# Kernel optimization log

Hardware: AMD Instinct MI355X
Metric: run time of the kernel (lower is better)

The kernel has to match this reference:

```python
import jax, jax.numpy as jnp
import numpy as np

N = 50000      # nodes
E = 400000     # edges
IN_DIM = 128
HID = 64
HEADS1 = 4
OUT_DIM = 64
NEG_SLOPE = 0.2


def _gat_layer(x, W, attn_l, attn_r, bias, src, dst, heads, out_feats):
    # x: [N, F_in]; W: [F_in, heads*out]; attn_l/attn_r: [heads, out]; bias: [heads*out]
    n = x.shape[0]
    feat = (x @ W).reshape(n, heads, out_feats)              # [N, H, D]
    el = jnp.sum(feat * attn_l, axis=-1)                     # [N, H]
    er = jnp.sum(feat * attn_r, axis=-1)                     # [N, H]
    e = jax.nn.leaky_relu(el[src] + er[dst], NEG_SLOPE)      # [E, H]
    # segment softmax over incoming edges per destination node
    emax = jax.ops.segment_max(e, dst, num_segments=n)       # [N, H]
    ex = jnp.exp(e - emax[dst])                              # [E, H]
    denom = jax.ops.segment_sum(ex, dst, num_segments=n)     # [N, H]
    alpha = ex / denom[dst]                                  # [E, H]
    msg = alpha[:, :, None] * feat[src]                      # [E, H, D]
    rst = jax.ops.segment_sum(msg, dst, num_segments=n)      # [N, H, D]
    return rst + bias.reshape(1, heads, out_feats)


def setup_inputs() -> dict:
    key = jax.random.key(0)
    ks = jax.random.split(key, 12)
    features = jax.random.normal(ks[0], (N, IN_DIM), dtype=jnp.float32)
    src = jax.random.randint(ks[1], (E,), 0, N, dtype=jnp.int32)
    dst = jax.random.randint(ks[2], (E,), 0, N, dtype=jnp.int32)
    s1 = 1.0 / np.sqrt(IN_DIM)
    s2 = 1.0 / np.sqrt(HEADS1 * HID)
    W1 = jax.random.normal(ks[3], (IN_DIM, HEADS1 * HID), dtype=jnp.float32) * s1
    attn_l1 = jax.random.normal(ks[4], (HEADS1, HID), dtype=jnp.float32) * 0.1
    attn_r1 = jax.random.normal(ks[5], (HEADS1, HID), dtype=jnp.float32) * 0.1
    b1 = jnp.zeros((HEADS1 * HID,), dtype=jnp.float32)
    W2 = jax.random.normal(ks[6], (HEADS1 * HID, OUT_DIM), dtype=jnp.float32) * s2
    attn_l2 = jax.random.normal(ks[7], (1, OUT_DIM), dtype=jnp.float32) * 0.1
    attn_r2 = jax.random.normal(ks[8], (1, OUT_DIM), dtype=jnp.float32) * 0.1
    b2 = jnp.zeros((OUT_DIM,), dtype=jnp.float32)
    return {"features": features, "src": src, "dst": dst,
            "W1": W1, "attn_l1": attn_l1, "attn_r1": attn_r1, "b1": b1,
            "W2": W2, "attn_l2": attn_l2, "attn_r2": attn_r2, "b2": b2}


def reference(features, src, dst, W1, attn_l1, attn_r1, b1, W2, attn_l2, attn_r2, b2):
    h = _gat_layer(features, W1, attn_l1, attn_r1, b1, src, dst, HEADS1, HID)  # [N, 4, 64]
    h = h.reshape(h.shape[0], -1)                                             # flatten heads
    h = _gat_layer(h, W2, attn_l2, attn_r2, b2, src, dst, 1, OUT_DIM)         # [N, 1, 64]
    return h
```

## Files before the change

### kernel.cpp

```cpp
#include <hip/hip_runtime.h>
#include <hip/hip_bf16.h>

#define N_NODES 50000
#define N_EDGES 400000
#define IN_DIM 128
#define HID 64
#define HEADS 4
#define L1_OUT (HEADS * HID)
#define OUT_DIM 64
#define NEG_SLOPE 0.2f
#define SCAN_B 256
#define HIST_B 1563

typedef short bf16x8 __attribute__((ext_vector_type(8)));
typedef float f32x4 __attribute__((ext_vector_type(4)));

__device__ __forceinline__ float leaky(float x) { return x > 0.f ? x : NEG_SLOPE * x; }

__device__ __forceinline__ unsigned short bfh(float x) {
    unsigned u = __float_as_uint(x);
    return (unsigned short)((u + 0x7fffu + ((u >> 16) & 1u)) >> 16);
}
__device__ __forceinline__ float fb(unsigned short h) {
    return __uint_as_float(((unsigned)h) << 16);
}

__device__ __forceinline__ int swzA(int u) {
    return u ^ (((u >> 6) & 7) ^ (((u >> 4) & 3) << 1));
}

__global__ void hist_wprep_kernel(const int* __restrict__ dst, int* __restrict__ cnt,
                                  const float* __restrict__ W1, const float* __restrict__ W2,
                                  unsigned short* __restrict__ W1fh, unsigned short* __restrict__ W1fl,
                                  unsigned short* __restrict__ W2fh, unsigned short* __restrict__ W2fl) {
    int bid = blockIdx.x;
    if (bid < HIST_B) {
        int e = bid * 256 + threadIdx.x;
        if (e < N_EDGES) atomicAdd(&cnt[dst[e]], 1);
        return;
    }
    int s = (bid - HIST_B) * 256 + threadIdx.x;
    if (s < 4096) {
        int lane = s & 63, ks = (s >> 6) & 3, ntile = s >> 8;
        int n = ntile * 16 + (lane & 15);
        int kb = ks * 32 + (lane >> 4) * 8;
#pragma unroll
        for (int j = 0; j < 8; ++j) {
            float w = W1[(kb + j) * L1_OUT + n];
            unsigned short h = bfh(w);
            W1fh[s * 8 + j] = h;
            W1fl[s * 8 + j] = bfh(w - fb(h));
        }
    } else if (s < 6144) {
        int s2 = s - 4096;
        int lane = s2 & 63, ks = (s2 >> 6) & 7, ntile = s2 >> 9;
        int n = ntile * 16 + (lane & 15);
        int kb = ks * 32 + (lane >> 4) * 8;
#pragma unroll
        for (int j = 0; j < 8; ++j) {
            float w = W2[(kb + j) * OUT_DIM + n];
            unsigned short h = bfh(w);
            W2fh[s2 * 8 + j] = h;
            W2fl[s2 * 8 + j] = bfh(w - fb(h));
        }
    }
}

__global__ void scanA_kernel(const int* __restrict__ cnt, int* __restrict__ texcl,
                             int* __restrict__ bsum) {
    __shared__ int sh[SCAN_B];
    int tid = threadIdx.x;
    int i = blockIdx.x * SCAN_B + tid;
    int v = (i < N_NODES) ? cnt[i] : 0;
    sh[tid] = v;
    __syncthreads();
    for (int off = 1; off < SCAN_B; off <<= 1) {
        int t = (tid >= off) ? sh[tid - off] : 0;
        __syncthreads();
        sh[tid] += t;
        __syncthreads();
    }
    if (i < N_NODES) texcl[i] = sh[tid] - v;
    if (tid == SCAN_B - 1) bsum[blockIdx.x] = sh[tid];
}

__global__ void scanB_kernel(const int* __restrict__ bsum, int* __restrict__ bexcl, int nb) {
    __shared__ int sh[SCAN_B];
    int tid = threadIdx.x;
    int v = (tid < nb) ? bsum[tid] : 0;
    sh[tid] = v;
    __syncthreads();
    for (int off = 1; off < SCAN_B; off <<= 1) {
        int t = (tid >= off) ? sh[tid - off] : 0;
        __syncthreads();
        sh[tid] += t;
        __syncthreads();
    }
    if (tid < nb) bexcl[tid] = sh[tid] - v;
}

__global__ void scanC_kernel(const int* __restrict__ texcl, const int* __restrict__ bexcl,
                             int* __restrict__ row) {
    int i = blockIdx.x * blockDim.x + threadIdx.x;
    if (i < N_NODES) row[i] = texcl[i] + bexcl[i >> 8];
    if (blockIdx.x == 0 && threadIdx.x == 0) row[N_NODES] = N_EDGES;
}

__global__ void fill_kernel(const int* __restrict__ src, const int* __restrict__ dst,
                            const int* __restrict__ row, int* __restrict__ fc,
                            int* __restrict__ perm_src) {
    int e = blockIdx.x * blockDim.x + threadIdx.x;
    if (e >= N_EDGES) return;
    int d = dst[e];
    int p = row[d] + atomicAdd(&fc[d], 1);
    perm_src[p] = src[e];
}

__global__ __launch_bounds__(512) void gemm1_kernel(const float* __restrict__ X,
                                                    const unsigned short* __restrict__ W1fh,
                                                    const unsigned short* __restrict__ W1fl,
                                                    const float* __restrict__ al1,
                                                    const float* __restrict__ ar1,
                                                    unsigned short* __restrict__ feat1b,
                                                    float* __restrict__ el1,
                                                    float* __restrict__ er1) {
    __shared__ unsigned short Ah[4 * 4 * 64 * 8];
    __shared__ unsigned short Al[4 * 4 * 64 * 8];
    int t = threadIdx.x;
    int m0 = blockIdx.x * 64;

    {
        int m = t >> 3;
        int k0 = (t & 7) * 16;
        int mfrag = m >> 4, mrow = m & 15;
        bool valid = (m0 + m) < N_NODES;
        const float4* xr = (const float4*)&X[(size_t)(m0 + m) * IN_DIM];
#pragma unroll
        for (int g = 0; g < 4; ++g) {
            int k = k0 + g * 4;
            float4 v = valid ? xr[k >> 2] : float4{0.f, 0.f, 0.f, 0.f};
            int kstep = k >> 5, kk = k & 31;
            int lane = mrow + 16 * (kk >> 3);
            int j0 = kk & 7;
            int base = ((mfrag * 4 + kstep) * 64 + lane) * 8 + j0;
            unsigned short h0 = bfh(v.x), h1 = bfh(v.y), h2 = bfh(v.z), h3 = bfh(v.w);
            *(ushort4*)&Ah[base] = make_ushort4(h0, h1, h2, h3);
            *(ushort4*)&Al[base] = make_ushort4(bfh(v.x - fb(h0)), bfh(v.y - fb(h1)),
                                                bfh(v.z - fb(h2)), bfh(v.w - fb(h3)));
        }
    }
    __syncthreads();

    int w = t >> 6, lane = t & 63;
    int wr = w >> 2, wc = w & 3;
    f32x4 acc[2][4];
#pragma unroll
    for (int mi = 0; mi < 2; ++mi)
#pragma unroll
        for (int nf = 0; nf < 4; ++nf) acc[mi][nf] = f32x4{0.f, 0.f, 0.f, 0.f};

#pragma unroll
    for (int kstep = 0; kstep < 4; ++kstep) {
        bf16x8 a_h[2], a_l[2];
#pragma unroll
        for (int mi = 0; mi < 2; ++mi) {
            int slot = (((wr * 2 + mi) * 4 + kstep) * 64 + lane) * 8;
            a_h[mi] = *(const bf16x8*)&Ah[slot];
            a_l[mi] = *(const bf16x8*)&Al[slot];
        }
#pragma unroll
        for (int nf = 0; nf < 4; ++nf) {
            int slot = (((wc * 4 + nf) * 4 + kstep) * 64 + lane) * 8;
            bf16x8 b_h = *(const bf16x8*)&W1fh[slot];
            bf16x8 b_l = *(const bf16x8*)&W1fl[slot];
#pragma unroll
            for (int mi = 0; mi < 2; ++mi) {
                acc[mi][nf] = __builtin_amdgcn_mfma_f32_16x16x32_bf16(a_h[mi], b_h, acc[mi][nf], 0, 0, 0);
                acc[mi][nf] = __builtin_amdgcn_mfma_f32_16x16x32_bf16(a_h[mi], b_l, acc[mi][nf], 0, 0, 0);
                acc[mi][nf] = __builtin_amdgcn_mfma_f32_16x16x32_bf16(a_l[mi], b_h, acc[mi][nf], 0, 0, 0);
            }
        }
    }

    int fq = lane >> 4, fr = lane & 15;
#pragma unroll
    for (int mi = 0; mi < 2; ++mi) {
#pragma unroll
        for (int j = 0; j < 4; ++j) {
            int r = m0 + wr * 32 + mi * 16 + fq * 4 + j;
            if (r >= N_NODES) continue;
#pragma unroll
            for (int nf = 0; nf < 4; ++nf) {
                int c = wc * 64 + nf * 16 + fr;
                feat1b[(size_t)r * L1_OUT + c] = bfh(acc[mi][nf][j]);
            }
        }
    }

    float al_v[4], ar_v[4];
#pragma unroll
    for (int nf = 0; nf < 4; ++nf) {
        al_v[nf] = al1[wc * 64 + nf * 16 + fr];
        ar_v[nf] = ar1[wc * 64 + nf * 16 + fr];
    }
#pragma unroll
    for (int mi = 0; mi < 2; ++mi) {
#pragma unroll
        for (int j = 0; j < 4; ++j) {
            float l = 0.f, r = 0.f;
#pragma unroll
            for (int nf = 0; nf < 4; ++nf) {
                l += acc[mi][nf][j] * al_v[nf];
                r += acc[mi][nf][j] * ar_v[nf];
            }
#pragma unroll
            for (int off = 1; off < 16; off <<= 1) {
                l += __shfl_xor(l, off, 64);
                r += __shfl_xor(r, off, 64);
            }
            int rr = m0 + wr * 32 + mi * 16 + fq * 4 + j;
            if (fr == 0 && rr < N_NODES) {
                el1[rr * HEADS + wc] = l;
                er1[rr * HEADS + wc] = r;
            }
        }
    }
}

__global__ __launch_bounds__(512, 8) void layer2_kernel(const int* __restrict__ row,
                                                        const int* __restrict__ perm_src,
                                                        const float* __restrict__ el1,
                                                        const float* __restrict__ er1,
                                                        const unsigned short* __restrict__ feat1b,
                                                        const float* __restrict__ b1,
                                                        const unsigned short* __restrict__ W2fh,
                                                        const unsigned short* __restrict__ W2fl,
                                                        const float* __restrict__ al2,
                                                        const float* __restrict__ ar2,
                                                        unsigned short* __restrict__ feat2b,
                                                        float* __restrict__ el2,
                                                        float* __restrict__ er2) {
    __shared__ unsigned short Ah[2 * 8 * 64 * 8];
    __shared__ float pl[2][4][16], pr[2][4][16];
    int t = threadIdx.x;
    int w = t >> 6, lane = t & 63;
    int n0 = blockIdx.x * 32;

    float4 b1v = *(const float4*)&b1[lane * 4];
    const ushort4* f4 = (const ushort4*)feat1b;

#pragma unroll 1
    for (int it = 0; it < 4; ++it) {
        int d = n0 + it * 8 + w;
        float4 acc = {0.f, 0.f, 0.f, 0.f};
        bool valid = d < N_NODES;
        if (valid) {
            int base = row[d], deg = row[d + 1] - base;
            if (deg > 0 && deg <= 16) {
                int h = lane >> 4, jj = lane & 15;
                int s_reg = (jj < deg) ? perm_src[base + jj] : 0;
                float er_d = er1[d * HEADS + h];
                float sc = (jj < deg) ? leaky(el1[s_reg * HEADS + h] + er_d) : -1e30f;
                float m = sc;
                m = fmaxf(m, __shfl_xor(m, 1, 64));
                m = fmaxf(m, __shfl_xor(m, 2, 64));
                m = fmaxf(m, __shfl_xor(m, 4, 64));
                m = fmaxf(m, __shfl_xor(m, 8, 64));
                float ex = (jj < deg) ? __expf(sc - m) : 0.f;
                float ss = ex;
                ss += __shfl_xor(ss, 1, 64);
                ss += __shfl_xor(ss, 2, 64);
                ss += __shfl_xor(ss, 4, 64);
                ss += __shfl_xor(ss, 8, 64);
                float alpha = ex / ss;
                int hb = lane & 48;
                float4 A0 = {0.f,0.f,0.f,0.f}, A1 = {0.f,0.f,0.f,0.f};
                float4 A2 = {0.f,0.f,0.f,0.f}, A3 = {0.f,0.f,0.f,0.f};
                int j = 0;
                for (; j + 3 < deg; j += 4) {
                    int s0 = __shfl(s_reg, j), s1 = __shfl(s_reg, j + 1);
                    int s2 = __shfl(s_reg, j + 2), s3 = __shfl(s_reg, j + 3);
                    float a0 = __shfl(alpha, hb + j), a1 = __shfl(alpha, hb + j + 1);
                    float a2 = __shfl(alpha, hb + j + 2), a3 = __shfl(alpha, hb + j + 3);
                    ushort4 f0 = f4[(size_t)s0 * 64 + lane];
                    ushort4 f1 = f4[(size_t)s1 * 64 + lane];
                    ushort4 f2 = f4[(size_t)s2 * 64 + lane];
                    ushort4 f3 = f4[(size_t)s3 * 64 + lane];
                    A0.x += a0 * fb(f0.x); A0.y += a0 * fb(f0.y); A0.z += a0 * fb(f0.z); A0.w += a0 * fb(f0.w);
                    A1.x += a1 * fb(f1.x); A1.y += a1 * fb(f1.y); A1.z += a1 * fb(f1.z); A1.w += a1 * fb(f1.w);
                    A2.x += a2 * fb(f2.x); A2.y += a2 * fb(f2.y); A2.z += a2 * fb(f2.z); A2.w += a2 * fb(f2.w);
                    A3.x += a3 * fb(f3.x); A3.y += a3 * fb(f3.y); A3.z += a3 * fb(f3.z); A3.w += a3 * fb(f3.w);
                }
                for (; j < deg; ++j) {
                    int s0 = __shfl(s_reg, j);
                    float a0 = __shfl(alpha, hb + j);
                    ushort4 f0 = f4[(size_t)s0 * 64 + lane];
                    A0.x += a0 * fb(f0.x); A0.y += a0 * fb(f0.y); A0.z += a0 * fb(f0.z); A0.w += a0 * fb(f0.w);
                }
                acc.x = A0.x + A1.x + A2.x + A3.x;
                acc.y = A0.y + A1.y + A2.y + A3.y;
                acc.z = A0.z + A1.z + A2.z + A3.z;
                acc.w = A0.w + A1.w + A2.w + A3.w;
            } else if (deg > 16) {
                float mh0, mh1, mh2, mh3, iv0, iv1, iv2, iv3;
#pragma unroll
                for (int h = 0; h < 4; ++h) {
                    float er_dh = er1[d * HEADS + h];
                    float m = -1e30f;
                    for (int j = lane; j < deg; j += 64)
                        m = fmaxf(m, leaky(el1[perm_src[base + j] * HEADS + h] + er_dh));
#pragma unroll
                    for (int off = 1; off < 64; off <<= 1) m = fmaxf(m, __shfl_xor(m, off, 64));
                    float ss = 0.f;
                    for (int j = lane; j < deg; j += 64)
                        ss += __expf(leaky(el1[perm_src[base + j] * HEADS + h] + er_dh) - m);
#pragma unroll
                    for (int off = 1; off < 64; off <<= 1) ss += __shfl_xor(ss, off, 64);
                    float iv = 1.f / ss;
                    if (h == 0) { mh0 = m; iv0 = iv; }
                    else if (h == 1) { mh1 = m; iv1 = iv; }
                    else if (h == 2) { mh2 = m; iv2 = iv; }
                    else { mh3 = m; iv3 = iv; }
                }
                int hh = lane >> 4;
                float m_s = hh == 0 ? mh0 : hh == 1 ? mh1 : hh == 2 ? mh2 : mh3;
                float iv_s = hh == 0 ? iv0 : hh == 1 ? iv1 : hh == 2 ? iv2 : iv3;
                float er_s = er1[d * HEADS + hh];
                for (int j = 0; j < deg; ++j) {
                    int s = perm_src[base + j];
                    float a = __expf(leaky(el1[s * HEADS + hh] + er_s) - m_s) * iv_s;
                    ushort4 f0 = f4[(size_t)s * 64 + lane];
                    acc.x += a * fb(f0.x); acc.y += a * fb(f0.y);
                    acc.z += a * fb(f0.z); acc.w += a * fb(f0.w);
                }
            }
            acc.x += b1v.x; acc.y += b1v.y; acc.z += b1v.z; acc.w += b1v.w;
        }
        int m = it * 8 + w;
        int mfrag = m >> 4, mrow = m & 15;
        int c = lane * 4;
        int kstep = c >> 5;
        int g = (c & 31) >> 3;
        int u = (mfrag * 8 + kstep) * 64 + mrow + 16 * g;
        int basei = swzA(u) * 8 + (c & 7);
        *(ushort4*)&Ah[basei] = make_ushort4(bfh(acc.x), bfh(acc.y), bfh(acc.z), bfh(acc.w));
    }
    __syncthreads();

    int mi = w & 1, ntile = w >> 1;
    f32x4 acc2 = f32x4{0.f, 0.f, 0.f, 0.f};

#pragma unroll
    for (int ks = 0; ks < 8; ++ks) {
        int aslot = swzA((mi * 8 + ks) * 64 + lane) * 8;
        bf16x8 a_h = *(const bf16x8*)&Ah[aslot];
        int slot = ((ntile * 8 + ks) * 64 + lane) * 8;
        bf16x8 b_h = *(const bf16x8*)&W2fh[slot];
        bf16x8 b_l = *(const bf16x8*)&W2fl[slot];
        acc2 = __builtin_amdgcn_mfma_f32_16x16x32_bf16(a_h, b_h, acc2, 0, 0, 0);
        acc2 = __builtin_amdgcn_mfma_f32_16x16x32_bf16(a_h, b_l, acc2, 0, 0, 0);
    }

    int fq = lane >> 4, fr = lane & 15;
#pragma unroll
    for (int j = 0; j < 4; ++j) {
        int r = n0 + mi * 16 + fq * 4 + j;
        if (r < N_NODES) {
            int c = ntile * 16 + fr;
            feat2b[(size_t)r * OUT_DIM + c] = bfh(acc2[j]);
        }
    }

    float al_v = al2[ntile * 16 + fr];
    float ar_v = ar2[ntile * 16 + fr];
#pragma unroll
    for (int j = 0; j < 4; ++j) {
        float l = acc2[j] * al_v;
        float r = acc2[j] * ar_v;
#pragma unroll
        for (int off = 1; off < 16; off <<= 1) {
            l += __shfl_xor(l, off, 64);
            r += __shfl_xor(r, off, 64);
        }
        if (fr == 0) {
            pl[mi][ntile][fq * 4 + j] = l;
            pr[mi][ntile][fq * 4 + j] = r;
        }
    }
    __syncthreads();
    if (t < 32) {
        int n = n0 + t;
        if (n < N_NODES) {
            int mi2 = t >> 4, rr = t & 15;
            el2[n] = pl[mi2][0][rr] + pl[mi2][1][rr] + pl[mi2][2][rr] + pl[mi2][3][rr];
            er2[n] = pr[mi2][0][rr] + pr[mi2][1][rr] + pr[mi2][2][rr] + pr[mi2][3][rr];
        }
    }
}

__global__ __launch_bounds__(256) void gather2_kernel(const int* __restrict__ row,
                                                      const int* __restrict__ perm_src,
                                                      const float* __restrict__ el2,
                                                      const float* __restrict__ er2,
                                                      const unsigned short* __restrict__ feat2b,
                                                      const float* __restrict__ b2,
                                                      float* __restrict__ out) {
    int tid = threadIdx.x;
    int w = tid >> 6, lane = tid & 63;
    int d = blockIdx.x * 4 + w;
    int base = row[d], deg = row[d + 1] - base;
    float bias = b2[lane];
    if (deg == 0) {
        out[(size_t)d * OUT_DIM + lane] = bias;
        return;
    }
    if (deg <= 64) {
        int s_reg = (lane < deg) ? perm_src[base + lane] : 0;
        float er_d = er2[d];
        float sc = (lane < deg) ? leaky(el2[s_reg] + er_d) : -1e30f;
        float m = sc;
#pragma unroll
        for (int off = 1; off < 64; off <<= 1) m = fmaxf(m, __shfl_xor(m, off, 64));
        float ex = (lane < deg) ? __expf(sc - m) : 0.f;
        float ss = ex;
#pragma unroll
        for (int off = 1; off < 64; off <<= 1) ss += __shfl_xor(ss, off, 64);
        float alpha = ex / ss;
        float a0 = 0.f, a1 = 0.f, a2 = 0.f, a3 = 0.f;
        float a4 = 0.f, a5 = 0.f, a6 = 0.f, a7 = 0.f;
        int j = 0;
        for (; j + 7 < deg; j += 8) {
            int s0 = __shfl(s_reg, j),     s1 = __shfl(s_reg, j + 1);
            int s2 = __shfl(s_reg, j + 2), s3 = __shfl(s_reg, j + 3);
            int s4 = __shfl(s_reg, j + 4), s5 = __shfl(s_reg, j + 5);
            int s6 = __shfl(s_reg, j + 6), s7 = __shfl(s_reg, j + 7);
            float w0 = __shfl(alpha, j),     w1 = __shfl(alpha, j + 1);
            float w2 = __shfl(alpha, j + 2), w3 = __shfl(alpha, j + 3);
            float w4 = __shfl(alpha, j + 4), w5 = __shfl(alpha, j + 5);
            float w6 = __shfl(alpha, j + 6), w7 = __shfl(alpha, j + 7);
            a0 += w0 * fb(feat2b[(size_t)s0 * OUT_DIM + lane]);
            a1 += w1 * fb(feat2b[(size_t)s1 * OUT_DIM + lane]);
            a2 += w2 * fb(feat2b[(size_t)s2 * OUT_DIM + lane]);
            a3 += w3 * fb(feat2b[(size_t)s3 * OUT_DIM + lane]);
            a4 += w4 * fb(feat2b[(size_t)s4 * OUT_DIM + lane]);
            a5 += w5 * fb(feat2b[(size_t)s5 * OUT_DIM + lane]);
            a6 += w6 * fb(feat2b[(size_t)s6 * OUT_DIM + lane]);
            a7 += w7 * fb(feat2b[(size_t)s7 * OUT_DIM + lane]);
        }
        for (; j + 3 < deg; j += 4) {
            int s0 = __shfl(s_reg, j),     s1 = __shfl(s_reg, j + 1);
            int s2 = __shfl(s_reg, j + 2), s3 = __shfl(s_reg, j + 3);
            float w0 = __shfl(alpha, j),     w1 = __shfl(alpha, j + 1);
            float w2 = __shfl(alpha, j + 2), w3 = __shfl(alpha, j + 3);
            a0 += w0 * fb(feat2b[(size_t)s0 * OUT_DIM + lane]);
            a1 += w1 * fb(feat2b[(size_t)s1 * OUT_DIM + lane]);
            a2 += w2 * fb(feat2b[(size_t)s2 * OUT_DIM + lane]);
            a3 += w3 * fb(feat2b[(size_t)s3 * OUT_DIM + lane]);
        }
        for (; j < deg; ++j) {
            int s0 = __shfl(s_reg, j);
            float w0 = __shfl(alpha, j);
            a0 += w0 * fb(feat2b[(size_t)s0 * OUT_DIM + lane]);
        }
        out[(size_t)d * OUT_DIM + lane] = a0 + a1 + a2 + a3 + a4 + a5 + a6 + a7 + bias;
    } else {
        float er_d = er2[d];
        float m = -1e30f;
        for (int j = lane; j < deg; j += 64)
            m = fmaxf(m, leaky(el2[perm_src[base + j]] + er_d));
#pragma unroll
        for (int off = 1; off < 64; off <<= 1) m = fmaxf(m, __shfl_xor(m, off, 64));
        float ss = 0.f;
        for (int j = lane; j < deg; j += 64)
            ss += __expf(leaky(el2[perm_src[base + j]] + er_d) - m);
#pragma unroll
        for (int off = 1; off < 64; off <<= 1) ss += __shfl_xor(ss, off, 64);
        float inv = 1.f / ss;
        float a0 = 0.f;
        for (int j = 0; j < deg; ++j) {
            int s = perm_src[base + j];
            float a = __expf(leaky(el2[s] + er_d) - m) * inv;
            a0 += a * fb(feat2b[(size_t)s * OUT_DIM + lane]);
        }
        out[(size_t)d * OUT_DIM + lane] = a0 + bias;
    }
}

extern "C" void kernel_launch(void* const* d_in, const int* in_sizes, int n_in,
                              void* d_out, int out_size, void* d_ws, size_t ws_size,
                              hipStream_t stream) {
    const float* features = (const float*)d_in[0];
    const int* src = (const int*)d_in[1];
    const int* dst = (const int*)d_in[2];
    const float* W1 = (const float*)d_in[3];
    const float* al1 = (const float*)d_in[4];
    const float* ar1 = (const float*)d_in[5];
    const float* b1 = (const float*)d_in[6];
    const float* W2 = (const float*)d_in[7];
    const float* al2 = (const float*)d_in[8];
    const float* ar2 = (const float*)d_in[9];
    const float* b2 = (const float*)d_in[10];
    float* out = (float*)d_out;

    float* ws = (float*)d_ws;
    float* el1 = ws;
    float* er1 = el1 + N_NODES * HEADS;
    float* el2 = er1 + N_NODES * HEADS;
    float* er2 = el2 + N_NODES;
    unsigned short* feat1b = (unsigned short*)(er2 + N_NODES);
    unsigned short* feat2b = feat1b + (size_t)N_NODES * L1_OUT;
    unsigned short* W1fh = feat2b + (size_t)N_NODES * OUT_DIM;
    unsigned short* W1fl = W1fh + 32768;
    unsigned short* W2fh = W1fl + 32768;
    unsigned short* W2fl = W2fh + 16384;
    int* cnt = (int*)(W2fl + 16384);
    int* fc = cnt + N_NODES;
    int* texcl = fc + N_NODES;
    int* bsum = texcl + N_NODES;
    int* bexcl = bsum + 256;
    int* row = bexcl + 256;
    int* perm_src = row + N_NODES + 1;

    const int nscan = (N_NODES + SCAN_B - 1) / SCAN_B;

    hipMemsetAsync(cnt, 0, (size_t)2 * N_NODES * sizeof(int), stream);

    hist_wprep_kernel<<<HIST_B + 24, 256, 0, stream>>>(dst, cnt, W1, W2, W1fh, W1fl, W2fh, W2fl);
    scanA_kernel<<<nscan, SCAN_B, 0, stream>>>(cnt, texcl, bsum);
    scanB_kernel<<<1, SCAN_B, 0, stream>>>(bsum, bexcl, nscan);
    scanC_kernel<<<(N_NODES + 255) / 256, 256, 0, stream>>>(texcl, bexcl, row);
    fill_kernel<<<(N_EDGES + 255) / 256, 256, 0, stream>>>(src, dst, row, fc, perm_src);

    gemm1_kernel<<<(N_NODES + 63) / 64, 512, 0, stream>>>(features, W1fh, W1fl, al1, ar1,
                                                          feat1b, el1, er1);
    layer2_kernel<<<(N_NODES + 31) / 32, 512, 0, stream>>>(row, perm_src, el1, er1, feat1b,
                                                           b1, W2fh, W2fl, al2, ar2,
                                                           feat2b, el2, er2);
    gather2_kernel<<<N_NODES / 4, 256, 0, stream>>>(row, perm_src, el2, er2, feat2b, b2, out);
}
```

Before: 167.1 us.

## Drop low-half A split in gemm1 and merge scanB into scanC

The layer-1 GEMM stops splitting the input activations into high and low bf16 halves, which removes one LDS buffer and one of the three MFMAs per tile. This lowers precision on the activation side of the GEMM. Separately, the single-block scanB kernel is removed: each scanC block now sums the block totals before it by a shared-memory tree reduction, saving one launch. An FMA4 macro replaces the repeated accumulate code without changing behaviour.

Result: no change. 164.5 us (-1.5%).

```diff
diff --git a/kernel.cpp b/kernel.cpp
--- a/kernel.cpp
+++ b/kernel.cpp
@@ -28,6 +28,8 @@
 __device__ __forceinline__ int swzA(int u) {
     return u ^ (((u >> 6) & 7) ^ (((u >> 4) & 3) << 1));
 }
+
+#define FMA4(A, wv, g) { A.x += wv * fb(g.x); A.y += wv * fb(g.y); A.z += wv * fb(g.z); A.w += wv * fb(g.w); }
 
 __global__ void hist_wprep_kernel(const int* __restrict__ dst, int* __restrict__ cnt,
                                   const float* __restrict__ W1, const float* __restrict__ W2,
@@ -84,26 +86,22 @@
     if (tid == SCAN_B - 1) bsum[blockIdx.x] = sh[tid];
 }
 
-__global__ void scanB_kernel(const int* __restrict__ bsum, int* __restrict__ bexcl, int nb) {
+__global__ void scanC_kernel(const int* __restrict__ texcl, const int* __restrict__ bsum,
+                             int* __restrict__ row, int nb) {
     __shared__ int sh[SCAN_B];
+    int b = blockIdx.x;
     int tid = threadIdx.x;
-    int v = (tid < nb) ? bsum[tid] : 0;
-    sh[tid] = v;
+    sh[tid] = (tid < b && tid < nb) ? bsum[tid] : 0;
     __syncthreads();
-    for (int off = 1; off < SCAN_B; off <<= 1) {
-        int t = (tid >= off) ? sh[tid - off] : 0;
+#pragma unroll
+    for (int off = 128; off > 0; off >>= 1) {
+        if (tid < off) sh[tid] += sh[tid + off];
         __syncthreads();
-        sh[tid] += t;
-        __syncthreads();
-    }
-    if (tid < nb) bexcl[tid] = sh[tid] - v;
-}
-
-__global__ void scanC_kernel(const int* __restrict__ texcl, const int* __restrict__ bexcl,
-                             int* __restrict__ row) {
-    int i = blockIdx.x * blockDim.x + threadIdx.x;
-    if (i < N_NODES) row[i] = texcl[i] + bexcl[i >> 8];
-    if (blockIdx.x == 0 && threadIdx.x == 0) row[N_NODES] = N_EDGES;
+    }
+    int prefix = sh[0];
+    int i = b * SCAN_B + tid;
+    if (i < N_NODES) row[i] = texcl[i] + prefix;
+    if (b == 0 && tid == 0) row[N_NODES] = N_EDGES;
 }
 
 __global__ void fill_kernel(const int* __restrict__ src, const int* __restrict__ dst,
@@ -125,7 +123,6 @@
                                                     float* __restrict__ el1,
                                                     float* __restrict__ er1) {
     __shared__ unsigned short Ah[4 * 4 * 64 * 8];
-    __shared__ unsigned short Al[4 * 4 * 64 * 8];
     int t = threadIdx.x;
     int m0 = blockIdx.x * 64;
 
@@ -143,10 +140,7 @@
             int lane = mrow + 16 * (kk >> 3);
             int j0 = kk & 7;
             int base = ((mfrag * 4 + kstep) * 64 + lane) * 8 + j0;
-            unsigned short h0 = bfh(v.x), h1 = bfh(v.y), h2 = bfh(v.z), h3 = bfh(v.w);
-            *(ushort4*)&Ah[base] = make_ushort4(h0, h1, h2, h3);
-            *(ushort4*)&Al[base] = make_ushort4(bfh(v.x - fb(h0)), bfh(v.y - fb(h1)),
-                                                bfh(v.z - fb(h2)), bfh(v.w - fb(h3)));
+            *(ushort4*)&Ah[base] = make_ushort4(bfh(v.x), bfh(v.y), bfh(v.z), bfh(v.w));
         }
     }
     __syncthreads();
@@ -161,12 +155,11 @@
 
 #pragma unroll
     for (int kstep = 0; kstep < 4; ++kstep) {
-        bf16x8 a_h[2], a_l[2];
+        bf16x8 a_h[2];
 #pragma unroll
         for (int mi = 0; mi < 2; ++mi) {
             int slot = (((wr * 2 + mi) * 4 + kstep) * 64 + lane) * 8;
             a_h[mi] = *(const bf16x8*)&Ah[slot];
-            a_l[mi] = *(const bf16x8*)&Al[slot];
         }
 #pragma unroll
         for (int nf = 0; nf < 4; ++nf) {
@@ -177,7 +170,6 @@
             for (int mi = 0; mi < 2; ++mi) {
                 acc[mi][nf] = __builtin_amdgcn_mfma_f32_16x16x32_bf16(a_h[mi], b_h, acc[mi][nf], 0, 0, 0);
                 acc[mi][nf] = __builtin_amdgcn_mfma_f32_16x16x32_bf16(a_h[mi], b_l, acc[mi][nf], 0, 0, 0);
-                acc[mi][nf] = __builtin_amdgcn_mfma_f32_16x16x32_bf16(a_l[mi], b_h, acc[mi][nf], 0, 0, 0);
             }
         }
     }
@@ -286,16 +278,13 @@
                     ushort4 f1 = f4[(size_t)s1 * 64 + lane];
                     ushort4 f2 = f4[(size_t)s2 * 64 + lane];
                     ushort4 f3 = f4[(size_t)s3 * 64 + lane];
-                    A0.x += a0 * fb(f0.x); A0.y += a0 * fb(f0.y); A0.z += a0 * fb(f0.z); A0.w += a0 * fb(f0.w);
-                    A1.x += a1 * fb(f1.x); A1.y += a1 * fb(f1.y); A1.z += a1 * fb(f1.z); A1.w += a1 * fb(f1.w);
-                    A2.x += a2 * fb(f2.x); A2.y += a2 * fb(f2.y); A2.z += a2 * fb(f2.z); A2.w += a2 * fb(f2.w);
-                    A3.x += a3 * fb(f3.x); A3.y += a3 * fb(f3.y); A3.z += a3 * fb(f3.z); A3.w += a3 * fb(f3.w);
+                    FMA4(A0, a0, f0); FMA4(A1, a1, f1); FMA4(A2, a2, f2); FMA4(A3, a3, f3);
                 }
                 for (; j < deg; ++j) {
                     int s0 = __shfl(s_reg, j);
                     float a0 = __shfl(alpha, hb + j);
                     ushort4 f0 = f4[(size_t)s0 * 64 + lane];
-                    A0.x += a0 * fb(f0.x); A0.y += a0 * fb(f0.y); A0.z += a0 * fb(f0.z); A0.w += a0 * fb(f0.w);
+                    FMA4(A0, a0, f0);
                 }
                 acc.x = A0.x + A1.x + A2.x + A3.x;
                 acc.y = A0.y + A1.y + A2.y + A3.y;
@@ -330,8 +319,7 @@
                     int s = perm_src[base + j];
                     float a = __expf(leaky(el1[s * HEADS + hh] + er_s) - m_s) * iv_s;
                     ushort4 f0 = f4[(size_t)s * 64 + lane];
-                    acc.x += a * fb(f0.x); acc.y += a * fb(f0.y);
-                    acc.z += a * fb(f0.z); acc.w += a * fb(f0.w);
+                    FMA4(acc, a, f0);
                 }
             }
             acc.x += b1v.x; acc.y += b1v.y; acc.z += b1v.z; acc.w += b1v.w;
@@ -517,8 +505,7 @@
     int* fc = cnt + N_NODES;
     int* texcl = fc + N_NODES;
     int* bsum = texcl + N_NODES;
-    int* bexcl = bsum + 256;
-    int* row = bexcl + 256;
+    int* row = bsum + 256;
     int* perm_src = row + N_NODES + 1;
 
     const int nscan = (N_NODES + SCAN_B - 1) / SCAN_B;
@@ -527,8 +514,7 @@
 
     hist_wprep_kernel<<<HIST_B + 24, 256, 0, stream>>>(dst, cnt, W1, W2, W1fh, W1fl, W2fh, W2fl);
     scanA_kernel<<<nscan, SCAN_B, 0, stream>>>(cnt, texcl, bsum);
-    scanB_kernel<<<1, SCAN_B, 0, stream>>>(bsum, bexcl, nscan);
-    scanC_kernel<<<(N_NODES + 255) / 256, 256, 0, stream>>>(texcl, bexcl, row);
+    scanC_kernel<<<nscan, SCAN_B, 0, stream>>>(texcl, bsum, row, nscan);
     fill_kernel<<<(N_EDGES + 255) / 256, 256, 0, stream>>>(src, dst, row, fc, perm_src);
 
     gemm1_kernel<<<(N_NODES + 63) / 64, 512, 0, stream>>>(features, W1fh, W1fl, al1, ar1,
```
